# Performance work log

Measured on AMD Instinct MI355X. Metric: run time of the kernel, lower is better.

The kernel has to match this reference:

```python
import jax, jax.numpy as jnp
import numpy as np

EMBED_DIM = 256
NUM_HEADS = 8
HEAD_DIM = EMBED_DIM // NUM_HEADS
NUM_POINTS_LIST = [4, 4, 4, 4]
PT = sum(NUM_POINTS_LIST)  # 16 points per head, total_points = 8*16 = 128
OFFSET_SCALE = 0.5
SHAPES = np.array([[128, 128], [64, 64], [32, 32], [16, 16]], dtype=np.int32)
BS, LQ = 8, 1000


def setup_inputs() -> dict:
    key = jax.random.key(0)
    ks = jax.random.split(key, 12)
    Lv = int((SHAPES[:, 0] * SHAPES[:, 1]).sum())  # 21760
    C = EMBED_DIM
    s = 0.02
    return {
        "query": jax.random.normal(ks[0], (BS, LQ, C), jnp.float32),
        "reference_points": jax.random.uniform(ks[1], (BS, LQ, 1, 4), jnp.float32, 0.1, 0.9),
        "value": jax.random.normal(ks[2], (BS, Lv, C), jnp.float32),
        "spatial_shapes": SHAPES,  # static numpy, not traced
        "w_off": jax.random.normal(ks[3], (C, NUM_HEADS * PT * 2), jnp.float32) * s,
        "b_off": jax.random.normal(ks[4], (NUM_HEADS * PT * 2,), jnp.float32) * 0.5,
        "w_attn": jax.random.normal(ks[5], (C, NUM_HEADS * PT), jnp.float32) * s,
        "b_attn": jnp.zeros((NUM_HEADS * PT,), jnp.float32),
        "w_val": jax.random.normal(ks[6], (C, C), jnp.float32) * s,
        "b_val": jnp.zeros((C,), jnp.float32),
        "w_out": jax.random.normal(ks[7], (C, C), jnp.float32) * s,
        "b_out": jnp.zeros((C,), jnp.float32),
    }


def _sample_level(v, loc, H, W):
    """Bilinear sample (grid_sample, align_corners=False, zero padding).
    v:   [bs, nH, H*W, hd]  value features of one pyramid level
    loc: [bs, Lq, nH, P, 2] sampling locations in [0,1] (x, y)
    returns [bs, Lq, nH, P, hd]
    """
    bs, Lq, nH, P, _ = loc.shape
    hd = v.shape[-1]
    x = loc[..., 0] * W - 0.5
    y = loc[..., 1] * H - 0.5
    x0 = jnp.floor(x)
    y0 = jnp.floor(y)
    lx = x - x0
    ly = y - y0
    x0i = x0.astype(jnp.int32)
    y0i = y0.astype(jnp.int32)

    def corner(xi, yi, w):
        valid = (xi >= 0) & (xi < W) & (yi >= 0) & (yi < H)
        idx = jnp.clip(yi, 0, H - 1) * W + jnp.clip(xi, 0, W - 1)  # [bs,Lq,nH,P]
        idxf = jnp.transpose(idx, (0, 2, 1, 3)).reshape(bs, nH, Lq * P)
        g = jnp.take_along_axis(v, idxf[..., None], axis=2)  # [bs,nH,Lq*P,hd]
        wv = jnp.where(valid, w, 0.0).astype(v.dtype)
        wf = jnp.transpose(wv, (0, 2, 1, 3)).reshape(bs, nH, Lq * P, 1)
        return g * wf

    out = (corner(x0i, y0i, (1 - lx) * (1 - ly))
           + corner(x0i + 1, y0i, lx * (1 - ly))
           + corner(x0i, y0i + 1, (1 - lx) * ly)
           + corner(x0i + 1, y0i + 1, lx * ly))
    out = out.reshape(bs, nH, Lq, P, hd)
    return jnp.transpose(out, (0, 2, 1, 3, 4))


def reference(query, reference_points, value, spatial_shapes,
              w_off, b_off, w_attn, b_attn, w_val, b_val, w_out, b_out):
    shapes = np.asarray(spatial_shapes)  # static
    bs, Lq, C = query.shape
    Lv = value.shape[1]
    nH, hd, Pt = NUM_HEADS, HEAD_DIM, PT

    # value projection -> [bs, nH, Lv, hd]
    v = value @ w_val + b_val
    v = jnp.transpose(v.reshape(bs, Lv, nH, hd), (0, 2, 1, 3))

    # sampling offsets and attention weights from query
    off = (query @ w_off + b_off).reshape(bs, Lq, nH, Pt, 2)
    aw = jax.nn.softmax((query @ w_attn + b_attn).reshape(bs, Lq, nH, Pt), axis=-1)

    # reference_points: [bs, Lq, 1, 4] boxes (cx, cy, w, h) in [0,1]
    nps = jnp.asarray([1.0 / n for n in NUM_POINTS_LIST for _ in range(n)],
                      dtype=query.dtype)[:, None]  # [Pt,1]
    loc = (reference_points[:, :, None, :, :2]
           + off * nps * reference_points[:, :, None, :, 2:] * OFFSET_SCALE)  # [bs,Lq,nH,Pt,2]

    samples = []
    v_start = 0
    p_start = 0
    for l, (H, W) in enumerate(shapes):
        H, W = int(H), int(W)
        P = NUM_POINTS_LIST[l]
        v_l = jax.lax.dynamic_slice_in_dim(v, v_start, H * W, axis=2)
        loc_l = loc[:, :, :, p_start:p_start + P, :]
        samples.append(_sample_level(v_l, loc_l, H, W))
        v_start += H * W
        p_start += P
    samples = jnp.concatenate(samples, axis=3)  # [bs,Lq,nH,Pt,hd]

    out = jnp.einsum('blhp,blhpd->blhd', aw, samples).reshape(bs, Lq, C)
    return out @ w_out + b_out
```

## Files before the change

### kernel.cpp

```cpp
#include <hip/hip_runtime.h>

typedef unsigned short ushort_t;
typedef short s16x8 __attribute__((ext_vector_type(8)));
typedef float f32x4 __attribute__((ext_vector_type(4)));
typedef unsigned int uint2_t __attribute__((ext_vector_type(2)));
typedef unsigned int uint4_t __attribute__((ext_vector_type(4)));

#define KDIM 256
#define BK 64
#define LDST 72
#define LV_TOTAL 21760
#define HL 696320
#define NQ 8000
#define VM_TILES2 680
#define QOA_BLOCKS 96
#define VPROJ_BLOCKS 672

__device__ inline unsigned short f2b(float f) {
  union { float f; unsigned u; } v; v.f = f;
  return (unsigned short)((v.u + 0x7fffu + ((v.u >> 16) & 1u)) >> 16);
}
__device__ inline float b2f(unsigned short h) {
  union { unsigned u; float f; } v; v.u = ((unsigned)h) << 16;
  return v.f;
}
__device__ inline unsigned pack_bf16x2(float lo, float hi) {
  union { float f; unsigned u; } a, b;
  a.f = lo; b.f = hi;
  return __builtin_amdgcn_perm(b.u + 0x8000u, a.u + 0x8000u, 0x07060302u);
}
__device__ inline unsigned short f2b_cheap(float f) {
  union { float f; unsigned u; } v; v.f = f;
  return (unsigned short)((v.u + 0x8000u) >> 16);
}

__global__ __launch_bounds__(256) void prep_weights(
    const float* __restrict__ w_off, const float* __restrict__ w_attn,
    const float* __restrict__ w_val, const float* __restrict__ w_out,
    const float* __restrict__ b_off, const float* __restrict__ b_attn,
    ushort_t* __restrict__ wt_val, ushort_t* __restrict__ wt_qoa,
    ushort_t* __restrict__ wt_out, float* __restrict__ bias_qoa,
    int* __restrict__ counters)
{
  int bid = blockIdx.x;
  int k = threadIdx.x;
  if (bid < 256) {
    int n = bid;
    wt_val[n*KDIM + k] = f2b(w_val[k*256 + n]);
  } else if (bid < 640) {
    int n = bid - 256;
    float v = (n < 256) ? w_off[k*256 + n] : w_attn[k*128 + (n - 256)];
    wt_qoa[n*KDIM + k] = f2b(v);
  } else if (bid < 896) {
    int n = bid - 640;
    wt_out[n*KDIM + k] = f2b(w_out[k*256 + n]);
  } else {
    if (k < 128) counters[k] = 0;
    for (int i = k; i < 384; i += 256)
      bias_qoa[i] = (i < 256) ? b_off[i] : b_attn[i - 256];
  }
}

__global__ __launch_bounds__(512) void merged_gemms(
    const float* __restrict__ value, const ushort_t* __restrict__ wt_val,
    const float* __restrict__ b_val, ushort_t* __restrict__ v_proj,
    const float* __restrict__ query, const ushort_t* __restrict__ wt_qoa,
    const float* __restrict__ bias_qoa, float* __restrict__ qoa,
    int* __restrict__ counters)
{
  __shared__ __align__(16) char smem[65536];
  __shared__ int s_mt;
  const int tid  = threadIdx.x;
  const int wave = tid >> 6;
  const int lane = tid & 63;
  const int lrow = lane & 15;
  const int quad = lane >> 4;

  if (blockIdx.x < QOA_BLOCKS) {
    ushort_t* sA = (ushort_t*)smem;
    ushort_t* sB = (ushort_t*)(smem + 256 * LDST * 2);
    const int m0 = (blockIdx.x % 32) * 256;
    const int n0 = (blockIdx.x / 32) * 128;
    const int M = NQ, N = 384;

    f32x4 acc[2][8];
    #pragma unroll
    for (int i = 0; i < 2; ++i)
      #pragma unroll
      for (int j = 0; j < 8; ++j) acc[i][j] = {0.f, 0.f, 0.f, 0.f};

    for (int kc = 0; kc < KDIM; kc += BK) {
      #pragma unroll
      for (int i = 0; i < 8; ++i) {
        int f   = tid + i * 512;
        int row = f >> 4;
        int c4  = f & 15;
        int gr  = m0 + row;
        float4 val = {0.f, 0.f, 0.f, 0.f};
        if (gr < M) val = *(const float4*)(query + (size_t)gr * KDIM + kc + c4 * 4);
        uint2_t t;
        t.x = pack_bf16x2(val.x, val.y);
        t.y = pack_bf16x2(val.z, val.w);
        *(uint2_t*)&sA[row * LDST + c4 * 4] = t;
      }
      #pragma unroll
      for (int i = 0; i < 2; ++i) {
        int f   = tid + i * 512;
        int row = f >> 3;
        int seg = f & 7;
        s16x8 v = *(const s16x8*)(wt_qoa + (size_t)(n0 + row) * KDIM + kc + seg * 8);
        *(s16x8*)&sB[row * LDST + seg * 8] = v;
      }
      __syncthreads();
      #pragma unroll
      for (int ki = 0; ki < BK; ki += 32) {
        int krow = ki + quad * 8;
        s16x8 af[2], bfr[8];
        #pragma unroll
        for (int mt = 0; mt < 2; ++mt)
          af[mt] = *(const s16x8*)&sA[(wave * 32 + mt * 16 + lrow) * LDST + krow];
        #pragma unroll
        for (int nt = 0; nt < 8; ++nt)
          bfr[nt] = *(const s16x8*)&sB[(nt * 16 + lrow) * LDST + krow];
        #pragma unroll
        for (int mt = 0; mt < 2; ++mt)
          #pragma unroll
          for (int nt = 0; nt < 8; ++nt)
            acc[mt][nt] = __builtin_amdgcn_mfma_f32_16x16x32_bf16(
                bfr[nt], af[mt], acc[mt][nt], 0, 0, 0);
      }
      __syncthreads();
    }
    #pragma unroll
    for (int mt = 0; mt < 2; ++mt) {
      const int gm = m0 + wave * 32 + mt * 16 + lrow;
      if (gm < M) {
        #pragma unroll
        for (int nt = 0; nt < 8; ++nt) {
          const int gn = n0 + nt * 16 + quad * 4;
          const float4 b4 = *(const float4*)(bias_qoa + gn);
          float4 o = {acc[mt][nt][0] + b4.x, acc[mt][nt][1] + b4.y,
                      acc[mt][nt][2] + b4.z, acc[mt][nt][3] + b4.w};
          *(float4*)(qoa + (size_t)gm * N + gn) = o;
        }
      }
    }
    return;
  }

  ushort_t* sB = (ushort_t*)smem;
  const int vbid = blockIdx.x - QOA_BLOCKS;
  const int half = vbid & 1;
  const int n0   = half * 128;

  {
    const ushort_t* src = wt_val + (size_t)n0 * KDIM;
    #pragma unroll
    for (int i = 0; i < 8; ++i) {
      int g   = tid + i * 512;
      int row = g >> 5;
      int c   = g & 31;
      s16x8 v = *(const s16x8*)(src + row * KDIM + c * 8);
      *(s16x8*)&sB[row * 256 + ((c ^ (row & 7)) * 8)] = v;
    }
  }
  __syncthreads();

  float bv[8];
  #pragma unroll
  for (int nt = 0; nt < 8; ++nt) bv[nt] = b_val[n0 + nt * 16 + lrow];

  const int swz = lrow & 7;

  while (true) {
    if (tid == 0) s_mt = atomicAdd(&counters[half * 64], 1);
    __syncthreads();
    const int mt = s_mt;
    if (mt >= VM_TILES2) break;
    const int m0 = mt * 256;
    const int bidx  = mt / 85;
    const int rbase = m0 - bidx * 21760;
    const float* arow0 = value + (size_t)(m0 + wave * 32 + lrow) * KDIM + quad * 8;
    const float* arow1 = arow0 + 16 * KDIM;

    f32x4 acc[2][8];
    #pragma unroll
    for (int m = 0; m < 2; ++m)
      #pragma unroll
      for (int nt = 0; nt < 8; ++nt) acc[m][nt] = {0.f, 0.f, 0.f, 0.f};

    float4 st[2][2][2];
    st[0][0][0] = *(const float4*)(arow0);
    st[0][0][1] = *(const float4*)(arow0 + 4);
    st[0][1][0] = *(const float4*)(arow1);
    st[0][1][1] = *(const float4*)(arow1 + 4);

    #pragma unroll
    for (int ks = 0; ks < 8; ++ks) {
      const int cur = ks & 1, nxt = cur ^ 1;
      if (ks < 7) {
        const float* p0 = arow0 + (ks + 1) * 32;
        const float* p1 = arow1 + (ks + 1) * 32;
        st[nxt][0][0] = *(const float4*)(p0);
        st[nxt][0][1] = *(const float4*)(p0 + 4);
        st[nxt][1][0] = *(const float4*)(p1);
        st[nxt][1][1] = *(const float4*)(p1 + 4);
      }
      s16x8 af[2];
      #pragma unroll
      for (int m = 0; m < 2; ++m) {
        union { uint4_t d; s16x8 v; } u;
        u.d.x = pack_bf16x2(st[cur][m][0].x, st[cur][m][0].y);
        u.d.y = pack_bf16x2(st[cur][m][0].z, st[cur][m][0].w);
        u.d.z = pack_bf16x2(st[cur][m][1].x, st[cur][m][1].y);
        u.d.w = pack_bf16x2(st[cur][m][1].z, st[cur][m][1].w);
        af[m] = u.v;
      }
      #pragma unroll
      for (int nt = 0; nt < 8; ++nt) {
        s16x8 bf = *(const s16x8*)&sB[(nt * 16 + lrow) * 256 +
                                      (((4 * ks + quad) ^ swz) * 8)];
        acc[0][nt] = __builtin_amdgcn_mfma_f32_16x16x32_bf16(af[0], bf, acc[0][nt], 0, 0, 0);
        acc[1][nt] = __builtin_amdgcn_mfma_f32_16x16x32_bf16(af[1], bf, acc[1][nt], 0, 0, 0);
      }
    }

    #pragma unroll
    for (int m = 0; m < 2; ++m) {
      int rl = rbase + wave * 32 + m * 16 + quad * 4;
      #pragma unroll
      for (int nt = 0; nt < 8; ++nt) {
        int gn = n0 + nt * 16 + lrow;
        int h  = gn >> 5;
        int d  = gn & 31;
        ushort_t* dst = v_proj + (size_t)(bidx * 8 + h) * HL + (size_t)rl * 32 + d;
        #pragma unroll
        for (int r = 0; r < 4; ++r)
          dst[r * 32] = f2b_cheap(acc[m][nt][r] + bv[nt]);
      }
    }
    __syncthreads();
  }
}

__global__ __launch_bounds__(256) void ms_deform_sample(
    const ushort_t* __restrict__ v,
    const float* __restrict__ qoa,
    const float* __restrict__ refp,
    float* __restrict__ outq)
{
  __shared__ float s_w[512];
  __shared__ int   s_i[512];
  const int bq  = blockIdx.x;
  const int b   = bq / 1000;
  const int tid = threadIdx.x;

  if (tid < 128) {
    const int p = tid & 15;
    const float* qrow = qoa + (size_t)bq * 384;
    float logit = qrow[256 + tid];
    float mx = logit;
    #pragma unroll
    for (int s = 8; s >= 1; s >>= 1) mx = fmaxf(mx, __shfl_xor(mx, s, 16));
    float e = __expf(logit - mx);
    float sum = e;
    #pragma unroll
    for (int s = 8; s >= 1; s >>= 1) sum += __shfl_xor(sum, s, 16);
    float aw = e / sum;

    float ox = qrow[tid * 2], oy = qrow[tid * 2 + 1];
    const float* rp = refp + (size_t)bq * 4;
    float rx = rp[0], ry = rp[1], rw = rp[2], rh = rp[3];
    const int lvl = p >> 2;
    const int HWs[4] = {128, 64, 32, 16};
    const int STs[4] = {0, 16384, 20480, 21504};
    int W = HWs[lvl], H = HWs[lvl], st = STs[lvl];
    float lx = rx + ox * 0.125f * rw;
    float ly = ry + oy * 0.125f * rh;
    float x = lx * (float)W - 0.5f;
    float y = ly * (float)H - 0.5f;
    float x0f = floorf(x), y0f = floorf(y);
    int x0 = (int)x0f, y0 = (int)y0f;
    float fx = x - x0f, fy = y - y0f;
    float wc[4] = {(1.f - fx) * (1.f - fy), fx * (1.f - fy),
                   (1.f - fx) * fy,         fx * fy};
    #pragma unroll
    for (int c = 0; c < 4; ++c) {
      int xi = x0 + (c & 1);
      int yi = y0 + (c >> 1);
      bool valid = (xi >= 0) && (xi < W) && (yi >= 0) && (yi < H);
      int xc = min(max(xi, 0), W - 1);
      int yc = min(max(yi, 0), H - 1);
      s_w[tid * 4 + c] = valid ? wc[c] * aw : 0.f;
      s_i[tid * 4 + c] = st + yc * W + xc;
    }
  }
  __syncthreads();

  const int h   = tid >> 5;
  const int l32 = tid & 31;
  const int grp = l32 >> 2;
  const int sub = l32 & 3;
  const ushort_t* vb = v + (size_t)(b * 8 + h) * HL + sub * 8;

  float wreg[8]; int ireg[8];
  #pragma unroll
  for (int i = 0; i < 8; ++i) {
    int j = h * 64 + i * 8 + grp;
    wreg[i] = s_w[j];
    ireg[i] = s_i[j];
  }
  s16x8 vv[8];
  #pragma unroll
  for (int i = 0; i < 8; ++i)
    vv[i] = *(const s16x8*)(vb + (size_t)ireg[i] * 32);

  float acc[8];
  #pragma unroll
  for (int d = 0; d < 8; ++d) acc[d] = 0.f;
  #pragma unroll
  for (int i = 0; i < 8; ++i)
    #pragma unroll
    for (int d = 0; d < 8; ++d)
      acc[d] += wreg[i] * b2f((ushort_t)vv[i][d]);

  #pragma unroll
  for (int m = 4; m <= 16; m <<= 1)
    #pragma unroll
    for (int d = 0; d < 8; ++d)
      acc[d] += __shfl_xor(acc[d], m);

  if (l32 < 4) {
    float* dst = outq + (size_t)bq * 256 + h * 32 + l32 * 8;
    float4 o0 = {acc[0], acc[1], acc[2], acc[3]};
    float4 o1 = {acc[4], acc[5], acc[6], acc[7]};
    *(float4*)dst = o0;
    *(float4*)(dst + 4) = o1;
  }
}

__global__ __launch_bounds__(256) void gemm_bf16(
    const float* __restrict__ A, const ushort_t* __restrict__ Bt,
    const float* __restrict__ bias, float* __restrict__ Cf,
    int M, int N)
{
  __shared__ ushort_t sA[128 * LDST];
  __shared__ ushort_t sB[64 * LDST];
  const int tid  = threadIdx.x;
  const int m0   = blockIdx.x * 128;
  const int n0   = blockIdx.y * 64;
  const int wave = tid >> 6;
  const int lane = tid & 63;
  const int lrow = lane & 15;
  const int quad = lane >> 4;

  f32x4 acc[2][4];
  #pragma unroll
  for (int i = 0; i < 2; ++i)
    #pragma unroll
    for (int j = 0; j < 4; ++j) acc[i][j] = {0.f, 0.f, 0.f, 0.f};

  for (int kc = 0; kc < KDIM; kc += BK) {
    #pragma unroll
    for (int i = 0; i < 8; ++i) {
      int f   = tid + i * 256;
      int row = f >> 4;
      int c4  = f & 15;
      int gr  = m0 + row;
      float4 val = {0.f, 0.f, 0.f, 0.f};
      if (gr < M) val = *(const float4*)(A + (size_t)gr * KDIM + kc + c4 * 4);
      uint2_t t;
      t.x = pack_bf16x2(val.x, val.y);
      t.y = pack_bf16x2(val.z, val.w);
      *(uint2_t*)&sA[row * LDST + c4 * 4] = t;
    }
    #pragma unroll
    for (int i = 0; i < 2; ++i) {
      int f   = tid + i * 256;
      int row = f >> 3;
      int seg = f & 7;
      s16x8 v = *(const s16x8*)(Bt + (size_t)(n0 + row) * KDIM + kc + seg * 8);
      *(s16x8*)&sB[row * LDST + seg * 8] = v;
    }
    __syncthreads();
    #pragma unroll
    for (int ki = 0; ki < BK; ki += 32) {
      int krow = ki + quad * 8;
      s16x8 af[2], bfr[4];
      #pragma unroll
      for (int mt = 0; mt < 2; ++mt)
        af[mt] = *(const s16x8*)&sA[(wave * 32 + mt * 16 + lrow) * LDST + krow];
      #pragma unroll
      for (int nt = 0; nt < 4; ++nt)
        bfr[nt] = *(const s16x8*)&sB[(nt * 16 + lrow) * LDST + krow];
      #pragma unroll
      for (int mt = 0; mt < 2; ++mt)
        #pragma unroll
        for (int nt = 0; nt < 4; ++nt)
          acc[mt][nt] = __builtin_amdgcn_mfma_f32_16x16x32_bf16(
              bfr[nt], af[mt], acc[mt][nt], 0, 0, 0);
    }
    __syncthreads();
  }
  #pragma unroll
  for (int mt = 0; mt < 2; ++mt) {
    const int gm = m0 + wave * 32 + mt * 16 + lrow;
    if (gm < M) {
      #pragma unroll
      for (int nt = 0; nt < 4; ++nt) {
        const int gn = n0 + nt * 16 + quad * 4;
        const float4 b4 = *(const float4*)(bias + gn);
        float4 o = {acc[mt][nt][0] + b4.x, acc[mt][nt][1] + b4.y,
                    acc[mt][nt][2] + b4.z, acc[mt][nt][3] + b4.w};
        *(float4*)(Cf + (size_t)gm * N + gn) = o;
      }
    }
  }
}

extern "C" void kernel_launch(void* const* d_in, const int* in_sizes, int n_in,
                              void* d_out, int out_size, void* d_ws, size_t ws_size,
                              hipStream_t stream) {
  const float* query  = (const float*)d_in[0];
  const float* refp   = (const float*)d_in[1];
  const float* value  = (const float*)d_in[2];
  const float* w_off  = (const float*)d_in[4];
  const float* b_off  = (const float*)d_in[5];
  const float* w_attn = (const float*)d_in[6];
  const float* b_attn = (const float*)d_in[7];
  const float* w_val  = (const float*)d_in[8];
  const float* b_val  = (const float*)d_in[9];
  const float* w_out  = (const float*)d_in[10];
  const float* b_out  = (const float*)d_in[11];
  float* out = (float*)d_out;

  char* ws = (char*)d_ws;
  const size_t WS_NEEDED = 110069760;
  if (ws_size < WS_NEEDED) return;
  ushort_t* wt_val   = (ushort_t*)(ws);
  ushort_t* wt_qoa   = (ushort_t*)(ws + 131072);
  ushort_t* wt_out   = (ushort_t*)(ws + 327680);
  float*    bias_qoa = (float*)   (ws + 458752);
  int*      counters = (int*)     (ws + 460288);
  ushort_t* v_proj   = (ushort_t*)(ws + 460800);
  float*    qoa      = (float*)   (ws + 89589760);
  float*    outq     = (float*)   (ws + 101877760);

  prep_weights<<<897, 256, 0, stream>>>(w_off, w_attn, w_val, w_out, b_off, b_attn,
                                        wt_val, wt_qoa, wt_out, bias_qoa, counters);
  merged_gemms<<<QOA_BLOCKS + VPROJ_BLOCKS, 512, 0, stream>>>(
      value, wt_val, b_val, v_proj, query, wt_qoa, bias_qoa, qoa, counters);
  ms_deform_sample<<<NQ, 256, 0, stream>>>(v_proj, qoa, refp, outq);
  gemm_bf16<<<dim3(63, 4), 256, 0, stream>>>(outq, wt_out, b_out, out, NQ, 256);
}
```

Before: 352.3 us.

## Map one query per wave in deform sampling and shrink output GEMM tiles

The sampling kernel now assigns one query to each wave, so a block covers four queries. Each wave computes its own softmax and bilinear weights in wave-local shared memory, which lets the block-wide barrier be replaced by an lgkmcnt wait. Each lane gathers 32 corners in four batches of eight, and only one xor-shuffle reduction step is needed instead of three. Separately, the output GEMM uses 64-row tiles, doubling the block count to fill more CUs, and drops the bounds checks because 8000 divides evenly by 64. The per-wave softmax and corner setup work increases, and relying on lgkmcnt alone instead of a barrier assumes shared-memory visibility within a wave.

Result: no change. 352.0 us (-0.1%).

```diff
diff --git a/kernel.cpp b/kernel.cpp
--- a/kernel.cpp
+++ b/kernel.cpp
@@ -249,89 +249,105 @@
     const float* __restrict__ refp,
     float* __restrict__ outq)
 {
-  __shared__ float s_w[512];
-  __shared__ int   s_i[512];
-  const int bq  = blockIdx.x;
-  const int b   = bq / 1000;
-  const int tid = threadIdx.x;
-
-  if (tid < 128) {
-    const int p = tid & 15;
-    const float* qrow = qoa + (size_t)bq * 384;
-    float logit = qrow[256 + tid];
-    float mx = logit;
-    #pragma unroll
-    for (int s = 8; s >= 1; s >>= 1) mx = fmaxf(mx, __shfl_xor(mx, s, 16));
-    float e = __expf(logit - mx);
-    float sum = e;
-    #pragma unroll
-    for (int s = 8; s >= 1; s >>= 1) sum += __shfl_xor(sum, s, 16);
-    float aw = e / sum;
-
-    float ox = qrow[tid * 2], oy = qrow[tid * 2 + 1];
-    const float* rp = refp + (size_t)bq * 4;
-    float rx = rp[0], ry = rp[1], rw = rp[2], rh = rp[3];
+  __shared__ float s_w[4][512];
+  __shared__ int   s_i[4][512];
+  const int tid  = threadIdx.x;
+  const int wave = tid >> 6;
+  const int l    = tid & 63;
+  const int bq   = blockIdx.x * 4 + wave;
+  const int b    = bq / 1000;
+
+  const float* qrow = qoa + (size_t)bq * 384;
+  const float* rp   = refp + (size_t)bq * 4;
+  const float rx = rp[0], ry = rp[1], rw = rp[2], rh = rp[3];
+
+  {
+    const int p   = l & 15;
     const int lvl = p >> 2;
     const int HWs[4] = {128, 64, 32, 16};
     const int STs[4] = {0, 16384, 20480, 21504};
-    int W = HWs[lvl], H = HWs[lvl], st = STs[lvl];
-    float lx = rx + ox * 0.125f * rw;
-    float ly = ry + oy * 0.125f * rh;
-    float x = lx * (float)W - 0.5f;
-    float y = ly * (float)H - 0.5f;
-    float x0f = floorf(x), y0f = floorf(y);
-    int x0 = (int)x0f, y0 = (int)y0f;
-    float fx = x - x0f, fy = y - y0f;
-    float wc[4] = {(1.f - fx) * (1.f - fy), fx * (1.f - fy),
-                   (1.f - fx) * fy,         fx * fy};
-    #pragma unroll
-    for (int c = 0; c < 4; ++c) {
-      int xi = x0 + (c & 1);
-      int yi = y0 + (c >> 1);
-      bool valid = (xi >= 0) && (xi < W) && (yi >= 0) && (yi < H);
-      int xc = min(max(xi, 0), W - 1);
-      int yc = min(max(yi, 0), H - 1);
-      s_w[tid * 4 + c] = valid ? wc[c] * aw : 0.f;
-      s_i[tid * 4 + c] = st + yc * W + xc;
-    }
-  }
-  __syncthreads();
-
-  const int h   = tid >> 5;
-  const int l32 = tid & 31;
-  const int grp = l32 >> 2;
-  const int sub = l32 & 3;
+    const int W = HWs[lvl], H = HWs[lvl], st = STs[lvl];
+
+    float lg0 = qrow[256 + l];
+    float lg1 = qrow[256 + 64 + l];
+    float m0 = lg0, m1 = lg1;
+    #pragma unroll
+    for (int s = 8; s >= 1; s >>= 1) {
+      m0 = fmaxf(m0, __shfl_xor(m0, s));
+      m1 = fmaxf(m1, __shfl_xor(m1, s));
+    }
+    float e0 = __expf(lg0 - m0), e1 = __expf(lg1 - m1);
+    float su0 = e0, su1 = e1;
+    #pragma unroll
+    for (int s = 8; s >= 1; s >>= 1) {
+      su0 += __shfl_xor(su0, s);
+      su1 += __shfl_xor(su1, s);
+    }
+    const float aw0 = e0 / su0, aw1 = e1 / su1;
+
+    #pragma unroll
+    for (int half = 0; half < 2; ++half) {
+      const int s = l + half * 64;
+      const float aw = half ? aw1 : aw0;
+      const float ox = qrow[2 * s], oy = qrow[2 * s + 1];
+      float x = (rx + ox * 0.125f * rw) * (float)W - 0.5f;
+      float y = (ry + oy * 0.125f * rh) * (float)H - 0.5f;
+      float x0f = floorf(x), y0f = floorf(y);
+      int x0 = (int)x0f, y0 = (int)y0f;
+      float fx = x - x0f, fy = y - y0f;
+      float wc[4] = {(1.f - fx) * (1.f - fy), fx * (1.f - fy),
+                     (1.f - fx) * fy,         fx * fy};
+      #pragma unroll
+      for (int c = 0; c < 4; ++c) {
+        int xi = x0 + (c & 1);
+        int yi = y0 + (c >> 1);
+        bool valid = (xi >= 0) && (xi < W) && (yi >= 0) && (yi < H);
+        int xc = min(max(xi, 0), W - 1);
+        int yc = min(max(yi, 0), H - 1);
+        s_w[wave][s * 4 + c] = valid ? wc[c] * aw : 0.f;
+        s_i[wave][s * 4 + c] = st + yc * W + xc;
+      }
+    }
+  }
+  asm volatile("s_waitcnt lgkmcnt(0)" ::: "memory");
+
+  const int h     = l >> 3;
+  const int sub   = (l >> 1) & 3;
+  const int cpair = l & 1;
   const ushort_t* vb = v + (size_t)(b * 8 + h) * HL + sub * 8;
-
-  float wreg[8]; int ireg[8];
-  #pragma unroll
-  for (int i = 0; i < 8; ++i) {
-    int j = h * 64 + i * 8 + grp;
-    wreg[i] = s_w[j];
-    ireg[i] = s_i[j];
-  }
-  s16x8 vv[8];
-  #pragma unroll
-  for (int i = 0; i < 8; ++i)
-    vv[i] = *(const s16x8*)(vb + (size_t)ireg[i] * 32);
 
   float acc[8];
   #pragma unroll
   for (int d = 0; d < 8; ++d) acc[d] = 0.f;
+
   #pragma unroll
-  for (int i = 0; i < 8; ++i)
-    #pragma unroll
-    for (int d = 0; d < 8; ++d)
-      acc[d] += wreg[i] * b2f((ushort_t)vv[i][d]);
+  for (int batch = 0; batch < 4; ++batch) {
+    float wgt[8]; int idx[8];
+    #pragma unroll
+    for (int u = 0; u < 8; ++u) {
+      const int slot = batch * 8 + u;
+      const int p  = slot >> 1;
+      const int c  = cpair * 2 + (slot & 1);
+      const int j  = h * 64 + p * 4 + c;
+      wgt[u] = s_w[wave][j];
+      idx[u] = s_i[wave][j];
+    }
+    s16x8 vv[8];
+    #pragma unroll
+    for (int u = 0; u < 8; ++u)
+      vv[u] = *(const s16x8*)(vb + (size_t)idx[u] * 32);
+    #pragma unroll
+    for (int u = 0; u < 8; ++u)
+      #pragma unroll
+      for (int d = 0; d < 8; ++d)
+        acc[d] += wgt[u] * b2f((ushort_t)vv[u][d]);
+  }
 
   #pragma unroll
-  for (int m = 4; m <= 16; m <<= 1)
-    #pragma unroll
-    for (int d = 0; d < 8; ++d)
-      acc[d] += __shfl_xor(acc[d], m);
-
-  if (l32 < 4) {
-    float* dst = outq + (size_t)bq * 256 + h * 32 + l32 * 8;
+  for (int d = 0; d < 8; ++d) acc[d] += __shfl_xor(acc[d], 1);
+
+  if (cpair == 0) {
+    float* dst = outq + (size_t)bq * 256 + h * 32 + sub * 8;
     float4 o0 = {acc[0], acc[1], acc[2], acc[3]};
     float4 o1 = {acc[4], acc[5], acc[6], acc[7]};
     *(float4*)dst = o0;
@@ -344,31 +360,27 @@
     const float* __restrict__ bias, float* __restrict__ Cf,
     int M, int N)
 {
-  __shared__ ushort_t sA[128 * LDST];
+  __shared__ ushort_t sA[64 * LDST];
   __shared__ ushort_t sB[64 * LDST];
   const int tid  = threadIdx.x;
-  const int m0   = blockIdx.x * 128;
+  const int m0   = blockIdx.x * 64;
   const int n0   = blockIdx.y * 64;
   const int wave = tid >> 6;
   const int lane = tid & 63;
   const int lrow = lane & 15;
   const int quad = lane >> 4;
 
-  f32x4 acc[2][4];
+  f32x4 acc[4];
   #pragma unroll
-  for (int i = 0; i < 2; ++i)
-    #pragma unroll
-    for (int j = 0; j < 4; ++j) acc[i][j] = {0.f, 0.f, 0.f, 0.f};
+  for (int j = 0; j < 4; ++j) acc[j] = {0.f, 0.f, 0.f, 0.f};
 
   for (int kc = 0; kc < KDIM; kc += BK) {
     #pragma unroll
-    for (int i = 0; i < 8; ++i) {
+    for (int i = 0; i < 4; ++i) {
       int f   = tid + i * 256;
       int row = f >> 4;
       int c4  = f & 15;
-      int gr  = m0 + row;
-      float4 val = {0.f, 0.f, 0.f, 0.f};
-      if (gr < M) val = *(const float4*)(A + (size_t)gr * KDIM + kc + c4 * 4);
+      float4 val = *(const float4*)(A + (size_t)(m0 + row) * KDIM + kc + c4 * 4);
       uint2_t t;
       t.x = pack_bf16x2(val.x, val.y);
       t.y = pack_bf16x2(val.z, val.w);
@@ -386,34 +398,26 @@
     #pragma unroll
     for (int ki = 0; ki < BK; ki += 32) {
       int krow = ki + quad * 8;
-      s16x8 af[2], bfr[4];
-      #pragma unroll
-      for (int mt = 0; mt < 2; ++mt)
-        af[mt] = *(const s16x8*)&sA[(wave * 32 + mt * 16 + lrow) * LDST + krow];
+      s16x8 af = *(const s16x8*)&sA[(wave * 16 + lrow) * LDST + krow];
+      s16x8 bfr[4];
       #pragma unroll
       for (int nt = 0; nt < 4; ++nt)
         bfr[nt] = *(const s16x8*)&sB[(nt * 16 + lrow) * LDST + krow];
       #pragma unroll
-      for (int mt = 0; mt < 2; ++mt)
-        #pragma unroll
-        for (int nt = 0; nt < 4; ++nt)
-          acc[mt][nt] = __builtin_amdgcn_mfma_f32_16x16x32_bf16(
-              bfr[nt], af[mt], acc[mt][nt], 0, 0, 0);
+      for (int nt = 0; nt < 4; ++nt)
+        acc[nt] = __builtin_amdgcn_mfma_f32_16x16x32_bf16(bfr[nt], af, acc[nt], 0, 0, 0);
     }
     __syncthreads();
   }
-  #pragma unroll
-  for (int mt = 0; mt < 2; ++mt) {
-    const int gm = m0 + wave * 32 + mt * 16 + lrow;
-    if (gm < M) {
-      #pragma unroll
-      for (int nt = 0; nt < 4; ++nt) {
-        const int gn = n0 + nt * 16 + quad * 4;
-        const float4 b4 = *(const float4*)(bias + gn);
-        float4 o = {acc[mt][nt][0] + b4.x, acc[mt][nt][1] + b4.y,
-                    acc[mt][nt][2] + b4.z, acc[mt][nt][3] + b4.w};
-        *(float4*)(Cf + (size_t)gm * N + gn) = o;
-      }
+  {
+    const int gm = m0 + wave * 16 + lrow;
+    #pragma unroll
+    for (int nt = 0; nt < 4; ++nt) {
+      const int gn = n0 + nt * 16 + quad * 4;
+      const float4 b4 = *(const float4*)(bias + gn);
+      float4 o = {acc[nt][0] + b4.x, acc[nt][1] + b4.y,
+                  acc[nt][2] + b4.z, acc[nt][3] + b4.w};
+      *(float4*)(Cf + (size_t)gm * N + gn) = o;
     }
   }
 }
@@ -450,6 +454,6 @@
                                         wt_val, wt_qoa, wt_out, bias_qoa, counters);
   merged_gemms<<<QOA_BLOCKS + VPROJ_BLOCKS, 512, 0, stream>>>(
       value, wt_val, b_val, v_proj, query, wt_qoa, bias_qoa, qoa, counters);
-  ms_deform_sample<<<NQ, 256, 0, stream>>>(v_proj, qoa, refp, outq);
-  gemm_bf16<<<dim3(63, 4), 256, 0, stream>>>(outq, wt_out, b_out, out, NQ, 256);
-}
+  ms_deform_sample<<<NQ / 4, 256, 0, stream>>>(v_proj, qoa, refp, outq);
+  gemm_bf16<<<dim3(125, 4), 256, 0, stream>>>(outq, wt_out, b_out, out, NQ, 256);
+}
```
